# Performance work log

Measured on AMD Instinct MI355X. Metric: run time of the kernel, lower is better.

The kernel has to match this reference:

```python
import jax, jax.numpy as jnp
import numpy as np

N = 50000   # nodes
E = 800000  # edges (avg degree 16)
F = 256     # in_feats
H = 4       # num_heads
D = 64      # out_feats per head (H*D == F)


def setup_inputs() -> dict:
    key = jax.random.key(0)
    ks = jax.random.split(key, 10)
    s = 0.02
    HD = H * D
    return {
        "feat": jax.random.normal(ks[0], (N, F), jnp.float32),
        "src": jax.random.randint(ks[1], (E,), 0, N),
        "dst": jax.random.randint(ks[2], (E,), 0, N),
        "Wq": jax.random.normal(ks[3], (HD, F), jnp.float32) * s,
        "bq": jnp.zeros((HD,), jnp.float32),
        "Wk": jax.random.normal(ks[4], (HD, F), jnp.float32) * s,
        "bk": jnp.zeros((HD,), jnp.float32),
        "Wv": jax.random.normal(ks[5], (HD, F), jnp.float32) * s,
        "bv": jnp.zeros((HD,), jnp.float32),
        "Wskip": jax.random.normal(ks[6], (HD, F), jnp.float32) * s,
        "bskip": jnp.zeros((HD,), jnp.float32),
        "Wgate": jax.random.normal(ks[7], (1, 3 * HD), jnp.float32) * s,
        "bgate": jnp.zeros((1,), jnp.float32),
        "ln_w": jnp.ones((HD,), jnp.float32),
        "ln_b": jnp.zeros((HD,), jnp.float32),
        "prelu_a": jnp.float32(0.25),
    }


def reference(feat, src, dst, Wq, bq, Wk, bk, Wv, bv, Wskip, bskip,
              Wgate, bgate, ln_w, ln_b, prelu_a):
    n = feat.shape[0]
    scale = 1.0 / np.sqrt(D).astype(np.float32)
    # projections: note DGL code names q from src nodes, k from dst nodes
    q = (feat @ Wq.T + bq).reshape(n, H, D)
    k = (feat @ Wk.T + bk).reshape(n, H, D)
    v = (feat @ Wv.T + bv).reshape(n, H, D)
    # per-edge scores: u_dot_v('ft','ft') = q[src] . k[dst], scaled
    e = jnp.einsum('ehd,ehd->eh', q[src], k[dst]) * scale  # [E, H]
    # edge softmax over incoming edges of each destination node
    m = jax.ops.segment_max(e, dst, num_segments=n)          # [N, H]
    ex = jnp.exp(e - m[dst])
    denom = jax.ops.segment_sum(ex, dst, num_segments=n)    # [N, H]
    sa = ex / denom[dst]                                     # [E, H]
    # weighted scatter-aggregate: sum_e sa * v[src]
    agg = jax.ops.segment_sum(sa[:, :, None] * v[src], dst, num_segments=n)
    rst = agg.reshape(n, H * D)
    # gated skip connection
    skip = feat @ Wskip.T + bskip
    g = jax.nn.sigmoid(
        jnp.concatenate([skip, rst, skip - rst], axis=-1) @ Wgate.T + bgate)
    rst = g * skip + (1.0 - g) * rst
    # layer norm
    mu = rst.mean(-1, keepdims=True)
    var = rst.var(-1, keepdims=True)
    rst = (rst - mu) * jax.lax.rsqrt(var + 1e-5) * ln_w + ln_b
    # PReLU
    return jnp.where(rst >= 0, rst, prelu_a * rst)
```

## Files before the change

### kernel.cpp

```cpp
#include <hip/hip_runtime.h>
#include <math.h>


typedef __attribute__((ext_vector_type(8))) short short8;
typedef __attribute__((ext_vector_type(4))) float floatx4;
typedef __attribute__((ext_vector_type(2))) float floatx2;
typedef __attribute__((address_space(3))) void lds_void;
typedef __attribute__((address_space(1))) const void gbl_void;

__device__ inline unsigned short f2bf(float x) {
    unsigned int u = __float_as_uint(x);
    u = (u + 0x7fffu + ((u >> 16) & 1u)) >> 16;
    return (unsigned short)u;
}
__device__ inline float bf2f(unsigned short u) {
    return __uint_as_float(((unsigned int)u) << 16);
}

__global__ void prep_kernel(const float* __restrict__ f, ushort* __restrict__ fb,
                            int n_elems, int total_pad,
                            const float* __restrict__ Wq, const float* __restrict__ Wk,
                            const float* __restrict__ Wv, const float* __restrict__ Wsk,
                            const float* __restrict__ bq, const float* __restrict__ bk,
                            const float* __restrict__ bv, const float* __restrict__ bsk,
                            ushort* __restrict__ Wcat, float* __restrict__ bcat,
                            int* __restrict__ counts, int* __restrict__ cursor, int n)
{
    int g = blockIdx.x * blockDim.x + threadIdx.x;
    int featQ = total_pad >> 2;
    if (g < featQ) {
        int i = g * 4;
        float4 v = (i < n_elems) ? *(const float4*)(f + i) : make_float4(0.f, 0.f, 0.f, 0.f);
        ushort4 u;
        u.x = f2bf(v.x); u.y = f2bf(v.y); u.z = f2bf(v.z); u.w = f2bf(v.w);
        *(ushort4*)(fb + i) = u;
        return;
    }
    int g2 = g - featQ;
    if (g2 < 65536) {
        int i = g2 * 4;
        int mat = i >> 16;
        int rem = i & 65535;
        const float* W = (mat == 0) ? Wq : (mat == 1) ? Wk : (mat == 2) ? Wv : Wsk;
        float4 v = *(const float4*)(W + rem);
        ushort4 u;
        u.x = f2bf(v.x); u.y = f2bf(v.y); u.z = f2bf(v.z); u.w = f2bf(v.w);
        *(ushort4*)(Wcat + i) = u;
        return;
    }
    int g3 = g2 - 65536;
    if (g3 < 256) {
        int o = g3 * 4;
        int mat = o >> 8;
        const float* b = (mat == 0) ? bq : (mat == 1) ? bk : (mat == 2) ? bv : bsk;
        *(float4*)(bcat + o) = *(const float4*)(b + (o & 255));
        return;
    }
    int g4 = g3 - 256;
    if (g4 < n) counts[g4] = 0;
    if (g4 == 0) *cursor = 0;
}


__global__ void count_kernel(const int* __restrict__ dst, int* counts, int e) {
    int i = blockIdx.x * blockDim.x + threadIdx.x;
    if (i < e) atomicAdd(&counts[dst[i]], 1);
}

__global__ void alloc_kernel(const int* __restrict__ counts, int* start, int* cur,
                             int* cursor, int n) {
    int i = blockIdx.x * blockDim.x + threadIdx.x;
    int lane = threadIdx.x & 63;
    int c = (i < n) ? counts[i] : 0;
    int incl = c;
#pragma unroll
    for (int d = 1; d < 64; d <<= 1) {
        int t = __shfl_up(incl, d);
        if (lane >= d) incl += t;
    }
    int waveTot = __shfl(incl, 63);
    int base = 0;
    if (lane == 63) base = atomicAdd(cursor, waveTot);
    base = __shfl(base, 63);
    if (i < n) {
        int s = base + incl - c;
        start[i] = s;
        cur[i] = s;
    }
}

__global__ void fill_kernel(const int* __restrict__ dst, const int* __restrict__ src,
                            int* cur, int* srclist, int e) {
    int i = blockIdx.x * blockDim.x + threadIdx.x;
    if (i < e) {
        int pos = atomicAdd(&cur[dst[i]], 1);
        srclist[pos] = src[i];
    }
}

__global__ __launch_bounds__(512) void mfma_gemm(
    const ushort* __restrict__ featb, const ushort* __restrict__ Wcat,
    const float* __restrict__ bcat,
    unsigned char* __restrict__ q8, ushort* __restrict__ kb,
    unsigned char* __restrict__ v8, ushort* __restrict__ sb, int n)
{
    __shared__ ushort At[128 * 32];
    __shared__ ushort Bt[256 * 32];
    int tid = threadIdx.x;
    int lane = tid & 63;
    int wv = tid >> 6;
    int ysel = blockIdx.x;
    int mBase = blockIdx.y * 128;
    int nBlk = ysel * 256;
    int mQuad = (wv & 1) * 64;
    int nQuad = (wv >> 1) * 64;

    floatx4 zero = {0.f, 0.f, 0.f, 0.f};
    floatx4 acc[4][4];
#pragma unroll
    for (int i = 0; i < 4; ++i)
#pragma unroll
        for (int j = 0; j < 4; ++j) acc[i][j] = zero;

    int rsel = lane & 15;
    int ksel = (lane >> 4) * 8;
    int lrow = lane >> 2;
    int lcol = (lane & 3) * 8;

    for (int k0 = 0; k0 < 256; k0 += 32) {
        {
            int row = 16 * wv + lrow;
            const ushort* gp = featb + (size_t)(mBase + row) * 256 + k0 + lcol;
            __builtin_amdgcn_global_load_lds((gbl_void*)gp, (lds_void*)&At[16 * wv * 32], 16, 0, 0);
        }
#pragma unroll
        for (int r = 0; r < 2; ++r) {
            int row = 32 * wv + 16 * r + lrow;
            const ushort* gp = Wcat + (size_t)(nBlk + row) * 256 + k0 + lcol;
            __builtin_amdgcn_global_load_lds((gbl_void*)gp, (lds_void*)&Bt[(32 * wv + 16 * r) * 32], 16, 0, 0);
        }
        __syncthreads();
        short8 af[4], bf[4];
#pragma unroll
        for (int i = 0; i < 4; ++i)
            af[i] = *(const short8*)&At[(mQuad + 16 * i + rsel) * 32 + ksel];
#pragma unroll
        for (int j = 0; j < 4; ++j)
            bf[j] = *(const short8*)&Bt[(nQuad + 16 * j + rsel) * 32 + ksel];
#pragma unroll
        for (int i = 0; i < 4; ++i)
#pragma unroll
            for (int j = 0; j < 4; ++j)
                acc[i][j] = __builtin_amdgcn_mfma_f32_16x16x32_bf16(bf[j], af[i], acc[i][j], 0, 0, 0);
        __syncthreads();
    }

    int rowq4 = (lane >> 4) * 4;
    float4 bias[4];
#pragma unroll
    for (int nt = 0; nt < 4; ++nt)
        bias[nt] = *(const float4*)(bcat + nBlk + nQuad + 16 * nt + rowq4);

    if (ysel == 0 || ysel == 2) {
        unsigned char* outp = (ysel == 0) ? q8 : v8;
#pragma unroll
        for (int mt = 0; mt < 4; ++mt) {
            int m = mBase + mQuad + 16 * mt + (lane & 15);
            if (m < n) {
                unsigned char* rowp = outp + (size_t)m * 256 + nQuad + rowq4;
#pragma unroll
                for (int nt = 0; nt < 4; ++nt) {
                    int pk = __builtin_amdgcn_cvt_pk_fp8_f32(
                        acc[mt][nt][0] + bias[nt].x, acc[mt][nt][1] + bias[nt].y, 0, false);
                    pk = __builtin_amdgcn_cvt_pk_fp8_f32(
                        acc[mt][nt][2] + bias[nt].z, acc[mt][nt][3] + bias[nt].w, pk, true);
                    *(int*)(rowp + 16 * nt) = pk;
                }
            }
        }
    } else {
        ushort* outp = (ysel == 1) ? kb : sb;
#pragma unroll
        for (int mt = 0; mt < 4; ++mt) {
            int m = mBase + mQuad + 16 * mt + (lane & 15);
            if (m < n) {
                ushort* rowp = outp + (size_t)m * 256 + nQuad + rowq4;
#pragma unroll
                for (int nt = 0; nt < 4; ++nt) {
                    uint lo = (uint)f2bf(acc[mt][nt][0] + bias[nt].x)
                            | ((uint)f2bf(acc[mt][nt][1] + bias[nt].y) << 16);
                    uint hi = (uint)f2bf(acc[mt][nt][2] + bias[nt].z)
                            | ((uint)f2bf(acc[mt][nt][3] + bias[nt].w) << 16);
                    *(uint2*)(rowp + 16 * nt) = make_uint2(lo, hi);
                }
            }
        }
    }
}

__global__ __launch_bounds__(256) void node_kernel(
    const unsigned char* __restrict__ q8, const ushort* __restrict__ kb,
    const unsigned char* __restrict__ v8, const ushort* __restrict__ sbuf,
    const int* __restrict__ srclist, const int* __restrict__ start,
    const int* __restrict__ counts,
    const float* __restrict__ Wg, const float* __restrict__ bg,
    const float* __restrict__ lnw, const float* __restrict__ lnb,
    const float* __restrict__ pa,
    float* __restrict__ out, int n, int E)
{
    int wvi = threadIdx.x >> 6;
    int lane = threadIdx.x & 63;
    int node = blockIdx.x * 4 + wvi;
    if (node >= n) return;

    int f0 = (lane >> 4) * 64 + (lane & 15) * 4;

    ushort4 ku = *(const ushort4*)(kb + (size_t)node * 256 + f0);
    float k0 = bf2f(ku.x), k1 = bf2f(ku.y), k2 = bf2f(ku.z), k3 = bf2f(ku.w);

    float lA = 0.f, a0 = 0.f, a1 = 0.f, a2 = 0.f, a3 = 0.f;
    float lB = 0.f, b0 = 0.f, b1 = 0.f, b2 = 0.f, b3 = 0.f;

    int sidx = start[node], cnt = counts[node];

    for (int base = 0; base < cnt; base += 64) {
        int m = min(64, cnt - base);
        int gi = sidx + base + lane;
        int batch = srclist[min(gi, E - 1)];
        int j = 0;
        for (; j + 1 < m; j += 2) {
            int s0i = __shfl(batch, j);
            int s1i = __shfl(batch, j + 1);
            uint qw0 = *(const uint*)(q8 + (size_t)s0i * 256 + f0);
            uint vw0 = *(const uint*)(v8 + (size_t)s0i * 256 + f0);
            uint qw1 = *(const uint*)(q8 + (size_t)s1i * 256 + f0);
            uint vw1 = *(const uint*)(v8 + (size_t)s1i * 256 + f0);
            floatx2 ql0 = __builtin_amdgcn_cvt_pk_f32_fp8(qw0, false);
            floatx2 qh0 = __builtin_amdgcn_cvt_pk_f32_fp8(qw0, true);
            floatx2 ql1 = __builtin_amdgcn_cvt_pk_f32_fp8(qw1, false);
            floatx2 qh1 = __builtin_amdgcn_cvt_pk_f32_fp8(qw1, true);
            float p0 = ql0[0] * k0 + ql0[1] * k1 + qh0[0] * k2 + qh0[1] * k3;
            float p1 = ql1[0] * k0 + ql1[1] * k1 + qh1[0] * k2 + qh1[1] * k3;
            p0 += __shfl_xor(p0, 1);  p1 += __shfl_xor(p1, 1);
            p0 += __shfl_xor(p0, 2);  p1 += __shfl_xor(p1, 2);
            p0 += __shfl_xor(p0, 4);  p1 += __shfl_xor(p1, 4);
            p0 += __shfl_xor(p0, 8);  p1 += __shfl_xor(p1, 8);
            float w0 = __expf(p0 * 0.125f);
            float w1 = __expf(p1 * 0.125f);
            floatx2 vl0 = __builtin_amdgcn_cvt_pk_f32_fp8(vw0, false);
            floatx2 vh0 = __builtin_amdgcn_cvt_pk_f32_fp8(vw0, true);
            floatx2 vl1 = __builtin_amdgcn_cvt_pk_f32_fp8(vw1, false);
            floatx2 vh1 = __builtin_amdgcn_cvt_pk_f32_fp8(vw1, true);
            lA += w0;
            a0 += w0 * vl0[0]; a1 += w0 * vl0[1];
            a2 += w0 * vh0[0]; a3 += w0 * vh0[1];
            lB += w1;
            b0 += w1 * vl1[0]; b1 += w1 * vl1[1];
            b2 += w1 * vh1[0]; b3 += w1 * vh1[1];
        }
        if (j < m) {
            int s0i = __shfl(batch, j);
            uint qw0 = *(const uint*)(q8 + (size_t)s0i * 256 + f0);
            uint vw0 = *(const uint*)(v8 + (size_t)s0i * 256 + f0);
            floatx2 ql0 = __builtin_amdgcn_cvt_pk_f32_fp8(qw0, false);
            floatx2 qh0 = __builtin_amdgcn_cvt_pk_f32_fp8(qw0, true);
            float p0 = ql0[0] * k0 + ql0[1] * k1 + qh0[0] * k2 + qh0[1] * k3;
            p0 += __shfl_xor(p0, 1);
            p0 += __shfl_xor(p0, 2);
            p0 += __shfl_xor(p0, 4);
            p0 += __shfl_xor(p0, 8);
            float w0 = __expf(p0 * 0.125f);
            floatx2 vl0 = __builtin_amdgcn_cvt_pk_f32_fp8(vw0, false);
            floatx2 vh0 = __builtin_amdgcn_cvt_pk_f32_fp8(vw0, true);
            lA += w0;
            a0 += w0 * vl0[0]; a1 += w0 * vl0[1];
            a2 += w0 * vh0[0]; a3 += w0 * vh0[1];
        }
    }
    float lsum = lA + lB;
    float inv = (lsum > 0.f) ? 1.f / lsum : 0.f;
    float r0 = (a0 + b0) * inv, r1 = (a1 + b1) * inv;
    float r2 = (a2 + b2) * inv, r3 = (a3 + b3) * inv;

    ushort4 su = *(const ushort4*)(sbuf + (size_t)node * 256 + f0);
    float s0 = bf2f(su.x), s1 = bf2f(su.y), s2 = bf2f(su.z), s3 = bf2f(su.w);

    float4 w0v = *(const float4*)(Wg + f0);
    float4 w1v = *(const float4*)(Wg + 256 + f0);
    float4 w2v = *(const float4*)(Wg + 512 + f0);
    float z = w0v.x * s0 + w0v.y * s1 + w0v.z * s2 + w0v.w * s3
            + w1v.x * r0 + w1v.y * r1 + w1v.z * r2 + w1v.w * r3
            + w2v.x * (s0 - r0) + w2v.y * (s1 - r1) + w2v.z * (s2 - r2) + w2v.w * (s3 - r3);
#pragma unroll
    for (int d = 32; d >= 1; d >>= 1) z += __shfl_xor(z, d);
    z += bg[0];
    float g = 1.f / (1.f + __expf(-z));

    float y0 = g * s0 + (1.f - g) * r0;
    float y1 = g * s1 + (1.f - g) * r1;
    float y2 = g * s2 + (1.f - g) * r2;
    float y3 = g * s3 + (1.f - g) * r3;

    float sum = y0 + y1 + y2 + y3;
#pragma unroll
    for (int d = 32; d >= 1; d >>= 1) sum += __shfl_xor(sum, d);
    float mu = sum * (1.f / 256.f);
    float d0 = y0 - mu, d1 = y1 - mu, d2 = y2 - mu, d3 = y3 - mu;
    float sq = d0 * d0 + d1 * d1 + d2 * d2 + d3 * d3;
#pragma unroll
    for (int d = 32; d >= 1; d >>= 1) sq += __shfl_xor(sq, d);
    float rstd = rsqrtf(sq * (1.f / 256.f) + 1e-5f);

    float4 lw = *(const float4*)(lnw + f0);
    float4 lb = *(const float4*)(lnb + f0);
    float o0 = d0 * rstd * lw.x + lb.x;
    float o1 = d1 * rstd * lw.y + lb.y;
    float o2 = d2 * rstd * lw.z + lb.z;
    float o3 = d3 * rstd * lw.w + lb.w;
    float ap = pa[0];
    o0 = (o0 >= 0.f) ? o0 : ap * o0;
    o1 = (o1 >= 0.f) ? o1 : ap * o1;
    o2 = (o2 >= 0.f) ? o2 : ap * o2;
    o3 = (o3 >= 0.f) ? o3 : ap * o3;

    *(float4*)(out + (size_t)node * 256 + f0) = make_float4(o0, o1, o2, o3);
}


extern "C" void kernel_launch(void* const* d_in, const int* in_sizes, int n_in,
                              void* d_out, int out_size, void* d_ws, size_t ws_size,
                              hipStream_t stream)
{
    const float* feat = (const float*)d_in[0];
    const int* src    = (const int*)d_in[1];
    const int* dst    = (const int*)d_in[2];
    const float* Wq   = (const float*)d_in[3];
    const float* bq   = (const float*)d_in[4];
    const float* Wk   = (const float*)d_in[5];
    const float* bk   = (const float*)d_in[6];
    const float* Wv   = (const float*)d_in[7];
    const float* bv   = (const float*)d_in[8];
    const float* Wsk  = (const float*)d_in[9];
    const float* bsk  = (const float*)d_in[10];
    const float* Wg   = (const float*)d_in[11];
    const float* bg   = (const float*)d_in[12];
    const float* lnw  = (const float*)d_in[13];
    const float* lnb  = (const float*)d_in[14];
    const float* pa   = (const float*)d_in[15];

    int N = in_sizes[0] / 256;
    int E = in_sizes[1];
    float* out = (float*)d_out;

    int Mtiles = (N + 127) / 128;
    int Npad = Mtiles * 128;

    char* ws = (char*)d_ws;
    size_t off = 0;
    auto alloc = [&](size_t bytes) { char* p = ws + off; off = (off + bytes + 255) & ~(size_t)255; return p; };
    ushort* featb      = (ushort*)alloc((size_t)Npad * 256 * 2);
    ushort* Wcat       = (ushort*)alloc(1024 * 256 * 2);
    float*  bcat       = (float*) alloc(1024 * 4);
    unsigned char* q8  = (unsigned char*)alloc((size_t)N * 256);
    unsigned char* v8  = (unsigned char*)alloc((size_t)N * 256);
    ushort* kb         = (ushort*)alloc((size_t)N * 256 * 2);
    ushort* sb         = (ushort*)alloc((size_t)N * 256 * 2);
    int* counts        = (int*)alloc((size_t)N * 4);
    int* startv        = (int*)alloc((size_t)N * 4);
    int* cur           = (int*)alloc((size_t)N * 4);
    int* cursor        = (int*)alloc(4);
    int* srclist       = (int*)alloc((size_t)E * 4);

    int totPad = Npad * 256;
    int prepThreads = totPad / 4 + 65536 + 256 + N;
    prep_kernel<<<(prepThreads + 255) / 256, 256, 0, stream>>>(
        feat, featb, N * 256, totPad, Wq, Wk, Wv, Wsk, bq, bk, bv, bsk,
        Wcat, bcat, counts, cursor, N);

    count_kernel<<<(E + 255) / 256, 256, 0, stream>>>(dst, counts, E);
    alloc_kernel<<<(N + 255) / 256, 256, 0, stream>>>(counts, startv, cur, cursor, N);
    fill_kernel<<<(E + 255) / 256, 256, 0, stream>>>(dst, src, cur, srclist, E);

    dim3 gg(4, Mtiles);
    mfma_gemm<<<gg, 512, 0, stream>>>(featb, Wcat, bcat, q8, kb, v8, sb, N);

    node_kernel<<<(N + 3) / 4, 256, 0, stream>>>(q8, kb, v8, sb, srclist, startv, counts,
                                                 Wg, bg, lnw, lnb, pa, out, N, E);
}
```

Measured before the change: 347.9 us.

## Split wave into two half-waves processing different edges with 8 features per lane

Each lane now covers 8 features with 8-byte loads, so a 32-lane half-wave spans one full node row, and the two half-waves process different edges at once (4 edges per iteration). Partial accumulators are merged across halves with a single xor-32 shuffle at the end. This widens the gather loads, shortens the per-edge head reductions, and raises the number of independent gathers in flight. The cost is more registers per lane and predicated work on the tail when the edge count is not a multiple of four.

```diff
diff --git a/kernel.cpp b/kernel.cpp
--- a/kernel.cpp
+++ b/kernel.cpp
@@ -213,117 +213,143 @@
     int node = blockIdx.x * 4 + wvi;
     if (node >= n) return;
 
-    int f0 = (lane >> 4) * 64 + (lane & 15) * 4;
-
-    ushort4 ku = *(const ushort4*)(kb + (size_t)node * 256 + f0);
-    float k0 = bf2f(ku.x), k1 = bf2f(ku.y), k2 = bf2f(ku.z), k3 = bf2f(ku.w);
-
-    float lA = 0.f, a0 = 0.f, a1 = 0.f, a2 = 0.f, a3 = 0.f;
-    float lB = 0.f, b0 = 0.f, b1 = 0.f, b2 = 0.f, b3 = 0.f;
+    int l32 = lane & 31;
+    int half = lane >> 5;
+    int f0 = l32 * 8;
+
+    short8 kv = *(const short8*)(kb + (size_t)node * 256 + f0);
+    float kf[8];
+#pragma unroll
+    for (int i = 0; i < 8; ++i) kf[i] = bf2f((unsigned short)kv[i]);
+
+    float acc[8];
+#pragma unroll
+    for (int i = 0; i < 8; ++i) acc[i] = 0.f;
+    float denom = 0.f;
 
     int sidx = start[node], cnt = counts[node];
 
     for (int base = 0; base < cnt; base += 64) {
         int m = min(64, cnt - base);
-        int gi = sidx + base + lane;
-        int batch = srclist[min(gi, E - 1)];
-        int j = 0;
-        for (; j + 1 < m; j += 2) {
-            int s0i = __shfl(batch, j);
-            int s1i = __shfl(batch, j + 1);
-            uint qw0 = *(const uint*)(q8 + (size_t)s0i * 256 + f0);
-            uint vw0 = *(const uint*)(v8 + (size_t)s0i * 256 + f0);
-            uint qw1 = *(const uint*)(q8 + (size_t)s1i * 256 + f0);
-            uint vw1 = *(const uint*)(v8 + (size_t)s1i * 256 + f0);
-            floatx2 ql0 = __builtin_amdgcn_cvt_pk_f32_fp8(qw0, false);
-            floatx2 qh0 = __builtin_amdgcn_cvt_pk_f32_fp8(qw0, true);
-            floatx2 ql1 = __builtin_amdgcn_cvt_pk_f32_fp8(qw1, false);
-            floatx2 qh1 = __builtin_amdgcn_cvt_pk_f32_fp8(qw1, true);
-            float p0 = ql0[0] * k0 + ql0[1] * k1 + qh0[0] * k2 + qh0[1] * k3;
-            float p1 = ql1[0] * k0 + ql1[1] * k1 + qh1[0] * k2 + qh1[1] * k3;
+        int batch = srclist[min(sidx + base + lane, E - 1)];
+        for (int j = 0; j < m; j += 4) {
+            int j0 = j + half;
+            int j1 = j0 + 2;
+            bool vld0 = j0 < m;
+            bool vld1 = j1 < m;
+            int s0 = __shfl(batch, vld0 ? j0 : j);
+            int s1 = __shfl(batch, vld1 ? j1 : j);
+            uint2 qw0 = *(const uint2*)(q8 + (size_t)s0 * 256 + f0);
+            uint2 vw0 = *(const uint2*)(v8 + (size_t)s0 * 256 + f0);
+            uint2 qw1 = *(const uint2*)(q8 + (size_t)s1 * 256 + f0);
+            uint2 vw1 = *(const uint2*)(v8 + (size_t)s1 * 256 + f0);
+
+            floatx2 qa0 = __builtin_amdgcn_cvt_pk_f32_fp8(qw0.x, false);
+            floatx2 qa1 = __builtin_amdgcn_cvt_pk_f32_fp8(qw0.x, true);
+            floatx2 qa2 = __builtin_amdgcn_cvt_pk_f32_fp8(qw0.y, false);
+            floatx2 qa3 = __builtin_amdgcn_cvt_pk_f32_fp8(qw0.y, true);
+            floatx2 qb0 = __builtin_amdgcn_cvt_pk_f32_fp8(qw1.x, false);
+            floatx2 qb1 = __builtin_amdgcn_cvt_pk_f32_fp8(qw1.x, true);
+            floatx2 qb2 = __builtin_amdgcn_cvt_pk_f32_fp8(qw1.y, false);
+            floatx2 qb3 = __builtin_amdgcn_cvt_pk_f32_fp8(qw1.y, true);
+
+            float p0 = qa0[0]*kf[0] + qa0[1]*kf[1] + qa1[0]*kf[2] + qa1[1]*kf[3]
+                     + qa2[0]*kf[4] + qa2[1]*kf[5] + qa3[0]*kf[6] + qa3[1]*kf[7];
+            float p1 = qb0[0]*kf[0] + qb0[1]*kf[1] + qb1[0]*kf[2] + qb1[1]*kf[3]
+                     + qb2[0]*kf[4] + qb2[1]*kf[5] + qb3[0]*kf[6] + qb3[1]*kf[7];
             p0 += __shfl_xor(p0, 1);  p1 += __shfl_xor(p1, 1);
             p0 += __shfl_xor(p0, 2);  p1 += __shfl_xor(p1, 2);
             p0 += __shfl_xor(p0, 4);  p1 += __shfl_xor(p1, 4);
-            p0 += __shfl_xor(p0, 8);  p1 += __shfl_xor(p1, 8);
-            float w0 = __expf(p0 * 0.125f);
-            float w1 = __expf(p1 * 0.125f);
-            floatx2 vl0 = __builtin_amdgcn_cvt_pk_f32_fp8(vw0, false);
-            floatx2 vh0 = __builtin_amdgcn_cvt_pk_f32_fp8(vw0, true);
-            floatx2 vl1 = __builtin_amdgcn_cvt_pk_f32_fp8(vw1, false);
-            floatx2 vh1 = __builtin_amdgcn_cvt_pk_f32_fp8(vw1, true);
-            lA += w0;
-            a0 += w0 * vl0[0]; a1 += w0 * vl0[1];
-            a2 += w0 * vh0[0]; a3 += w0 * vh0[1];
-            lB += w1;
-            b0 += w1 * vl1[0]; b1 += w1 * vl1[1];
-            b2 += w1 * vh1[0]; b3 += w1 * vh1[1];
+            float w0 = vld0 ? __expf(p0 * 0.125f) : 0.f;
+            float w1 = vld1 ? __expf(p1 * 0.125f) : 0.f;
+
+            floatx2 va0 = __builtin_amdgcn_cvt_pk_f32_fp8(vw0.x, false);
+            floatx2 va1 = __builtin_amdgcn_cvt_pk_f32_fp8(vw0.x, true);
+            floatx2 va2 = __builtin_amdgcn_cvt_pk_f32_fp8(vw0.y, false);
+            floatx2 va3 = __builtin_amdgcn_cvt_pk_f32_fp8(vw0.y, true);
+            floatx2 vb0 = __builtin_amdgcn_cvt_pk_f32_fp8(vw1.x, false);
+            floatx2 vb1 = __builtin_amdgcn_cvt_pk_f32_fp8(vw1.x, true);
+            floatx2 vb2 = __builtin_amdgcn_cvt_pk_f32_fp8(vw1.y, false);
+            floatx2 vb3 = __builtin_amdgcn_cvt_pk_f32_fp8(vw1.y, true);
+
+            denom += w0 + w1;
+            acc[0] = fmaf(w0, va0[0], fmaf(w1, vb0[0], acc[0]));
+            acc[1] = fmaf(w0, va0[1], fmaf(w1, vb0[1], acc[1]));
+            acc[2] = fmaf(w0, va1[0], fmaf(w1, vb1[0], acc[2]));
+            acc[3] = fmaf(w0, va1[1], fmaf(w1, vb1[1], acc[3]));
+            acc[4] = fmaf(w0, va2[0], fmaf(w1, vb2[0], acc[4]));
+            acc[5] = fmaf(w0, va2[1], fmaf(w1, vb2[1], acc[5]));
+            acc[6] = fmaf(w0, va3[0], fmaf(w1, vb3[0], acc[6]));
+            acc[7] = fmaf(w0, va3[1], fmaf(w1, vb3[1], acc[7]));
         }
-        if (j < m) {
-            int s0i = __shfl(batch, j);
-            uint qw0 = *(const uint*)(q8 + (size_t)s0i * 256 + f0);
-            uint vw0 = *(const uint*)(v8 + (size_t)s0i * 256 + f0);
-            floatx2 ql0 = __builtin_amdgcn_cvt_pk_f32_fp8(qw0, false);
-            floatx2 qh0 = __builtin_amdgcn_cvt_pk_f32_fp8(qw0, true);
-            float p0 = ql0[0] * k0 + ql0[1] * k1 + qh0[0] * k2 + qh0[1] * k3;
-            p0 += __shfl_xor(p0, 1);
-            p0 += __shfl_xor(p0, 2);
-            p0 += __shfl_xor(p0, 4);
-            p0 += __shfl_xor(p0, 8);
-            float w0 = __expf(p0 * 0.125f);
-            floatx2 vl0 = __builtin_amdgcn_cvt_pk_f32_fp8(vw0, false);
-            floatx2 vh0 = __builtin_amdgcn_cvt_pk_f32_fp8(vw0, true);
-            lA += w0;
-            a0 += w0 * vl0[0]; a1 += w0 * vl0[1];
-            a2 += w0 * vh0[0]; a3 += w0 * vh0[1];
-        }
-    }
-    float lsum = lA + lB;
-    float inv = (lsum > 0.f) ? 1.f / lsum : 0.f;
-    float r0 = (a0 + b0) * inv, r1 = (a1 + b1) * inv;
-    float r2 = (a2 + b2) * inv, r3 = (a3 + b3) * inv;
-
-    ushort4 su = *(const ushort4*)(sbuf + (size_t)node * 256 + f0);
-    float s0 = bf2f(su.x), s1 = bf2f(su.y), s2 = bf2f(su.z), s3 = bf2f(su.w);
-
-    float4 w0v = *(const float4*)(Wg + f0);
-    float4 w1v = *(const float4*)(Wg + 256 + f0);
-    float4 w2v = *(const float4*)(Wg + 512 + f0);
-    float z = w0v.x * s0 + w0v.y * s1 + w0v.z * s2 + w0v.w * s3
-            + w1v.x * r0 + w1v.y * r1 + w1v.z * r2 + w1v.w * r3
-            + w2v.x * (s0 - r0) + w2v.y * (s1 - r1) + w2v.z * (s2 - r2) + w2v.w * (s3 - r3);
-#pragma unroll
-    for (int d = 32; d >= 1; d >>= 1) z += __shfl_xor(z, d);
+    }
+
+#pragma unroll
+    for (int i = 0; i < 8; ++i) acc[i] += __shfl_xor(acc[i], 32);
+    denom += __shfl_xor(denom, 32);
+    float inv = (denom > 0.f) ? 1.f / denom : 0.f;
+    float r[8];
+#pragma unroll
+    for (int i = 0; i < 8; ++i) r[i] = acc[i] * inv;
+
+    short8 sv = *(const short8*)(sbuf + (size_t)node * 256 + f0);
+    float s[8];
+#pragma unroll
+    for (int i = 0; i < 8; ++i) s[i] = bf2f((unsigned short)sv[i]);
+
+    float4 wa0 = *(const float4*)(Wg + f0);
+    float4 wa1 = *(const float4*)(Wg + f0 + 4);
+    float4 wb0 = *(const float4*)(Wg + 256 + f0);
+    float4 wb1 = *(const float4*)(Wg + 256 + f0 + 4);
+    float4 wc0 = *(const float4*)(Wg + 512 + f0);
+    float4 wc1 = *(const float4*)(Wg + 512 + f0 + 4);
+    float z = wa0.x*s[0] + wa0.y*s[1] + wa0.z*s[2] + wa0.w*s[3]
+            + wa1.x*s[4] + wa1.y*s[5] + wa1.z*s[6] + wa1.w*s[7]
+            + wb0.x*r[0] + wb0.y*r[1] + wb0.z*r[2] + wb0.w*r[3]
+            + wb1.x*r[4] + wb1.y*r[5] + wb1.z*r[6] + wb1.w*r[7]
+            + wc0.x*(s[0]-r[0]) + wc0.y*(s[1]-r[1]) + wc0.z*(s[2]-r[2]) + wc0.w*(s[3]-r[3])
+            + wc1.x*(s[4]-r[4]) + wc1.y*(s[5]-r[5]) + wc1.z*(s[6]-r[6]) + wc1.w*(s[7]-r[7]);
+#pragma unroll
+    for (int d = 16; d >= 1; d >>= 1) z += __shfl_xor(z, d);
     z += bg[0];
     float g = 1.f / (1.f + __expf(-z));
 
-    float y0 = g * s0 + (1.f - g) * r0;
-    float y1 = g * s1 + (1.f - g) * r1;
-    float y2 = g * s2 + (1.f - g) * r2;
-    float y3 = g * s3 + (1.f - g) * r3;
-
-    float sum = y0 + y1 + y2 + y3;
-#pragma unroll
-    for (int d = 32; d >= 1; d >>= 1) sum += __shfl_xor(sum, d);
+    float y[8];
+#pragma unroll
+    for (int i = 0; i < 8; ++i) y[i] = g * s[i] + (1.f - g) * r[i];
+
+    float sum = y[0]+y[1]+y[2]+y[3]+y[4]+y[5]+y[6]+y[7];
+#pragma unroll
+    for (int d = 16; d >= 1; d >>= 1) sum += __shfl_xor(sum, d);
     float mu = sum * (1.f / 256.f);
-    float d0 = y0 - mu, d1 = y1 - mu, d2 = y2 - mu, d3 = y3 - mu;
-    float sq = d0 * d0 + d1 * d1 + d2 * d2 + d3 * d3;
-#pragma unroll
-    for (int d = 32; d >= 1; d >>= 1) sq += __shfl_xor(sq, d);
+    float dv[8];
+    float sq = 0.f;
+#pragma unroll
+    for (int i = 0; i < 8; ++i) { dv[i] = y[i] - mu; sq = fmaf(dv[i], dv[i], sq); }
+#pragma unroll
+    for (int d = 16; d >= 1; d >>= 1) sq += __shfl_xor(sq, d);
     float rstd = rsqrtf(sq * (1.f / 256.f) + 1e-5f);
 
-    float4 lw = *(const float4*)(lnw + f0);
-    float4 lb = *(const float4*)(lnb + f0);
-    float o0 = d0 * rstd * lw.x + lb.x;
-    float o1 = d1 * rstd * lw.y + lb.y;
-    float o2 = d2 * rstd * lw.z + lb.z;
-    float o3 = d3 * rstd * lw.w + lb.w;
+    float4 lw0 = *(const float4*)(lnw + f0);
+    float4 lw1 = *(const float4*)(lnw + f0 + 4);
+    float4 lb0 = *(const float4*)(lnb + f0);
+    float4 lb1 = *(const float4*)(lnb + f0 + 4);
+    float lwv[8] = {lw0.x, lw0.y, lw0.z, lw0.w, lw1.x, lw1.y, lw1.z, lw1.w};
+    float lbv[8] = {lb0.x, lb0.y, lb0.z, lb0.w, lb1.x, lb1.y, lb1.z, lb1.w};
     float ap = pa[0];
-    o0 = (o0 >= 0.f) ? o0 : ap * o0;
-    o1 = (o1 >= 0.f) ? o1 : ap * o1;
-    o2 = (o2 >= 0.f) ? o2 : ap * o2;
-    o3 = (o3 >= 0.f) ? o3 : ap * o3;
-
-    *(float4*)(out + (size_t)node * 256 + f0) = make_float4(o0, o1, o2, o3);
+    float o[8];
+#pragma unroll
+    for (int i = 0; i < 8; ++i) {
+        float t = dv[i] * rstd * lwv[i] + lbv[i];
+        o[i] = (t >= 0.f) ? t : ap * t;
+    }
+
+    float4 stv;
+    stv.x = half ? o[4] : o[0];
+    stv.y = half ? o[5] : o[1];
+    stv.z = half ? o[6] : o[2];
+    stv.w = half ? o[7] : o[3];
+    *(float4*)(out + (size_t)node * 256 + f0 + 4 * half) = stv;
 }
 
 
```

New measurement: 350.3 us. About the same (+0.7%).
